# Optimization experiments

Hardware: AMD Instinct MI355X
Metric: run time of the kernel (lower is better)

Reference implementation:

```python
import jax, jax.numpy as jnp
import numpy as np

SEMA_DIM = 1024
L1, L2, B = 256, 320, 64


def setup_inputs() -> dict:
    key = jax.random.key(0)
    k1, k2, kw1, kb1, kw2, kb2 = jax.random.split(key, 6)
    D = SEMA_DIM
    s = 1.0 / np.sqrt(D)
    return {
        "r1": jax.random.normal(k1, (L1, B, D), dtype=jnp.float32),
        "r2": jax.random.normal(k2, (L2, B, D), dtype=jnp.float32),
        "W1": jax.random.uniform(kw1, (D, D), jnp.float32, -s, s),
        "b1": jax.random.uniform(kb1, (D,), jnp.float32, -s, s),
        "W2": jax.random.uniform(kw2, (D, D), jnp.float32, -s, s),
        "b2": jax.random.uniform(kb2, (D,), jnp.float32, -s, s),
    }


def _mlp(x, W1, b1, W2, b2):
    # torch Linear: x @ W.T + b
    h = jax.nn.relu(x @ W1.T + b1)
    return h @ W2.T + b2


def reference(r1, r2, W1, b1, W2, b2):
    # (L, B, D) -> mlp -> (B, L, D)
    r1 = jnp.transpose(_mlp(r1, W1, b1, W2, b2), (1, 0, 2))  # [B, L1, D]
    r2 = jnp.transpose(_mlp(r2, W1, b1, W2, b2), (1, 0, 2))  # [B, L2, D]

    o = jnp.einsum("bid,bjd->bij", r1, r2)  # [B, L1, L2]
    o1 = jax.nn.softmax(o, axis=2)           # attend r1 -> r2
    o2 = jax.nn.softmax(o, axis=1)           # attend r2 -> r1

    r1_c = jnp.einsum("bij,bjd->bid", o1, r2)  # [B, L1, D]
    r2_c = jnp.einsum("bij,bid->bjd", o2, r1)  # [B, L2, D]

    r1_pool = jnp.concatenate([r1, r1_c], axis=-1).sum(axis=1) / r1.shape[1]  # [B, 2D]
    r2_pool = jnp.concatenate([r2, r2_c], axis=-1).sum(axis=1) / r2.shape[1]  # [B, 2D]
    return (r1_pool, r2_pool)
```

## Files before the change

kernel.cpp:

```cpp
#include <hip/hip_runtime.h>
#include <stdint.h>

#define L1C 256
#define L2C 320
#define BC  64
#define DC  1024

typedef __bf16 bf16_t;
typedef __bf16 bf16x8 __attribute__((ext_vector_type(8)));
typedef __bf16 bf16x4 __attribute__((ext_vector_type(4)));
typedef float  f32x4  __attribute__((ext_vector_type(4)));

__device__ __forceinline__ void gload16(const void* g, void* l) {
  __builtin_amdgcn_global_load_lds(
      (__attribute__((address_space(1))) void*)g,
      (__attribute__((address_space(3))) void*)l, 16, 0, 0);
}

__global__ __launch_bounds__(256)
void conv_kernel(const float* __restrict__ src, bf16_t* __restrict__ dst, int n4) {
  int i = blockIdx.x * 256 + threadIdx.x;
  const int stride = gridDim.x * 256;
  for (; i < n4; i += stride) {
    float4 v = ((const float4*)src)[i];
    bf16x4 o = { (__bf16)v.x, (__bf16)v.y, (__bf16)v.z, (__bf16)v.w };
    ((bf16x4*)dst)[i] = o;
  }
}

__global__ __launch_bounds__(256)
void w2t_kernel(const float* __restrict__ W2, bf16_t* __restrict__ W2T) {
  __shared__ float tile[32][33];
  const int tx = threadIdx.x & 31, ty = threadIdx.x >> 5;
  const int x0 = blockIdx.x * 32, y0 = blockIdx.y * 32;
#pragma unroll
  for (int k = 0; k < 32; k += 8)
    tile[ty + k][tx] = W2[(size_t)(y0 + ty + k) * 1024 + x0 + tx];
  __syncthreads();
#pragma unroll
  for (int k = 0; k < 32; k += 8)
    W2T[(size_t)(x0 + ty + k) * 1024 + y0 + tx] = (bf16_t)tile[tx][ty + k];
}

__global__ __launch_bounds__(256)
void wb_kernel(const float* __restrict__ W2, const float* __restrict__ b2,
               float* __restrict__ w2b) {
  const int dt = threadIdx.x & 15, kg = threadIdx.x >> 4;
  const int d = blockIdx.x * 16 + dt;
  float s = 0.f;
  for (int k = kg * 64; k < kg * 64 + 64; ++k)
    s += W2[(size_t)k * 1024 + d] * b2[k];
  __shared__ float red[16][17];
  red[kg][dt] = s;
  __syncthreads();
  if (kg == 0) {
    float t = 0.f;
#pragma unroll
    for (int g = 0; g < 16; ++g) t += red[g][dt];
    w2b[d] = t;
  }
}

__global__ __launch_bounds__(512, 2)
void mlp_gemm8(const bf16_t* __restrict__ A, const bf16_t* __restrict__ W,
               const float* __restrict__ bias, bf16_t* __restrict__ C,
               int Mtiles, int relu) {
  const int nwg = Mtiles * 4;
  const int cpx = nwg >> 3;
  const int wg  = ((int)blockIdx.x & 7) * cpx + ((int)blockIdx.x >> 3);
  const int mt = wg >> 2, nt = wg & 3;

  __shared__ __align__(16) char lds[131072];

  const int t    = threadIdx.x;
  const int lane = t & 63, wid = t >> 6;
  const int wm = wid >> 2, wn = wid & 3;
  const int rsel = lane & 15, hi = lane >> 4;
  const int t16 = t * 16;

  const int P0 = t16, P1 = 8192 + t16;
  const int Lg0 = P0 ^ ((P0 >> 3) & 0x30);
  const int Lg1 = P1 ^ ((P1 >> 3) & 0x30);
  const int rS0 = Lg0 >> 6, cS0 = (Lg0 & 63) >> 1;
  const int rS1 = Lg1 >> 6, cS1 = (Lg1 & 63) >> 1;
  const bf16_t* pA0 = A + (size_t)(mt * 256 + rS0) * 1024 + cS0;
  const bf16_t* pA1 = A + (size_t)(mt * 256 + rS1) * 1024 + cS1;
  const bf16_t* pB0 = W + (size_t)(nt * 256 + rS0) * 1024 + cS0;
  const bf16_t* pB1 = W + (size_t)(nt * 256 + rS1) * 1024 + cS1;

  const int kchunk = (hi ^ ((rsel >> 1) & 3)) << 4;
  const int offA = ((wm * 128 + rsel) << 6) + kchunk;
  const int offB = 16384 + ((wn * 64 + rsel) << 6) + kchunk;

  f32x4 acc[8][4] = {};
  bf16x8 bfr[4];

#pragma unroll
  for (int p = 0; p < 3; ++p) {
    char* db = lds + p * 32768;
    gload16(pA0 + p * 32, db + t16);
    gload16(pA1 + p * 32, db + 8192 + t16);
    gload16(pB0 + p * 32, db + 16384 + t16);
    gload16(pB1 + p * 32, db + 24576 + t16);
  }
  asm volatile("s_waitcnt vmcnt(8)" ::: "memory");
  __builtin_amdgcn_s_barrier();
  __builtin_amdgcn_sched_barrier(0);

#pragma unroll 1
  for (int tt = 0; tt < 32; ++tt) {
    const char* rb = lds + (tt & 3) * 32768;
    char* sb = lds + ((tt + 3) & 3) * 32768;
    const int ks = (tt + 3) * 32;
    bf16x8 af[4];
#pragma unroll
    for (int m = 0; m < 4; ++m) af[m] = *(const bf16x8*)(rb + offA + m * 1024);
#pragma unroll
    for (int n = 0; n < 4; ++n) bfr[n] = *(const bf16x8*)(rb + offB + n * 1024);
    if (tt < 29) {
      gload16(pA0 + ks, sb + t16);
      gload16(pA1 + ks, sb + 8192 + t16);
    }
    __builtin_amdgcn_s_setprio(1);
#pragma unroll
    for (int m = 0; m < 4; ++m)
#pragma unroll
      for (int n = 0; n < 4; ++n)
        acc[m][n] = __builtin_amdgcn_mfma_f32_16x16x32_bf16(af[m], bfr[n], acc[m][n], 0, 0, 0);
    __builtin_amdgcn_s_setprio(0);
    __builtin_amdgcn_s_barrier();
    __builtin_amdgcn_sched_barrier(0);
#pragma unroll
    for (int m = 0; m < 4; ++m) af[m] = *(const bf16x8*)(rb + offA + (m + 4) * 1024);
    if (tt < 29) {
      gload16(pB0 + ks, sb + 16384 + t16);
      gload16(pB1 + ks, sb + 24576 + t16);
    }
    __builtin_amdgcn_s_setprio(1);
#pragma unroll
    for (int m = 0; m < 4; ++m)
#pragma unroll
      for (int n = 0; n < 4; ++n)
        acc[m + 4][n] = __builtin_amdgcn_mfma_f32_16x16x32_bf16(af[m], bfr[n], acc[m + 4][n], 0, 0, 0);
    __builtin_amdgcn_s_setprio(0);
    if (tt < 29)       asm volatile("s_waitcnt vmcnt(8)" ::: "memory");
    else if (tt == 29) asm volatile("s_waitcnt vmcnt(4)" ::: "memory");
    else if (tt == 30) asm volatile("s_waitcnt vmcnt(0)" ::: "memory");
    __builtin_amdgcn_s_barrier();
    __builtin_amdgcn_sched_barrier(0);
  }

  const int row0 = mt * 256 + wm * 128 + hi * 4;
  const int col0 = nt * 256 + wn * 64 + rsel;
  float bv[4];
#pragma unroll
  for (int n = 0; n < 4; ++n) bv[n] = bias[col0 + n * 16];
#pragma unroll
  for (int m = 0; m < 8; ++m) {
#pragma unroll
    for (int q = 0; q < 4; ++q) {
      const size_t rr = (size_t)(row0 + m * 16 + q) * 1024;
#pragma unroll
      for (int n = 0; n < 4; ++n) {
        float v = acc[m][n][q] + bv[n];
        if (relu) v = fmaxf(v, 0.f);
        C[rr + col0 + n * 16] = (bf16_t)v;
      }
    }
  }
}

__global__ __launch_bounds__(256)
void mlp_gemm(const bf16_t* __restrict__ A, const bf16_t* __restrict__ W,
              const float* __restrict__ bias, bf16_t* __restrict__ C,
              int Mtiles, int relu) {
  const int nwg = Mtiles * 8;
  const int wg  = ((int)blockIdx.x & 7) * (nwg >> 3) + ((int)blockIdx.x >> 3);
  const int mt = wg >> 3, nt = wg & 7;

  const int f = threadIdx.x;
  const int lane = f & 63, w = f >> 6;
  const int sRow = f >> 2, sCol8 = (f & 3) * 8;

  const bf16_t* Ab = A + (size_t)mt * 128 * 1024 + (size_t)sRow * 1024 + sCol8;
  const bf16_t* Bb = W + (size_t)nt * 128 * 1024 + (size_t)sRow * 1024 + sCol8;

  __shared__ __align__(16) bf16_t sA[128 * 32];
  __shared__ __align__(16) bf16_t sB[128 * 32];
  bf16_t* sAp = sA + sRow * 32 + sCol8;
  bf16_t* sBp = sB + sRow * 32 + sCol8;

  const int wr = (w >> 1) * 64, wc = (w & 1) * 64;
  const int rsel = lane & 15, koff = (lane >> 4) * 8;
  const bf16_t* rA = sA + (wr + rsel) * 32 + koff;
  const bf16_t* rB = sB + (wc + rsel) * 32 + koff;

  f32x4 acc[4][4] = {};
  for (int kt = 0; kt < 1024; kt += 32) {
    __syncthreads();
    gload16(Ab + kt,             sAp);
    gload16(Ab + kt + 64 * 1024, sAp + 64 * 32);
    gload16(Bb + kt,             sBp);
    gload16(Bb + kt + 64 * 1024, sBp + 64 * 32);
    asm volatile("s_waitcnt vmcnt(0)" ::: "memory");
    __syncthreads();
    bf16x8 af[4], bfv[4];
#pragma unroll
    for (int m = 0; m < 4; ++m) af[m] = *(const bf16x8*)(rA + m * 16 * 32);
#pragma unroll
    for (int n = 0; n < 4; ++n) bfv[n] = *(const bf16x8*)(rB + n * 16 * 32);
#pragma unroll
    for (int m = 0; m < 4; ++m)
#pragma unroll
      for (int n = 0; n < 4; ++n)
        acc[m][n] = __builtin_amdgcn_mfma_f32_16x16x32_bf16(af[m], bfv[n], acc[m][n], 0, 0, 0);
  }

  const int row0 = mt * 128 + wr + (lane >> 4) * 4;
  const int col0 = nt * 128 + wc + rsel;
#pragma unroll
  for (int n = 0; n < 4; ++n) {
    const int c = col0 + n * 16;
    const float bv = bias[c];
#pragma unroll
    for (int m = 0; m < 4; ++m) {
      const int r = row0 + m * 16;
#pragma unroll
      for (int q = 0; q < 4; ++q) {
        float v = acc[m][n][q] + bv;
        if (relu) v = fmaxf(v, 0.f);
        C[(size_t)(r + q) * 1024 + c] = (bf16_t)v;
      }
    }
  }
}

__global__ __launch_bounds__(256)
void pool_gemm(const bf16_t* __restrict__ A, const bf16_t* __restrict__ W,
               const float* __restrict__ bias, float* __restrict__ out) {
  const int nwg = 16;
  const int wg  = ((int)blockIdx.x & 7) * (nwg >> 3) + ((int)blockIdx.x >> 3);
  const int mt = wg >> 3, nt = wg & 7;

  const int f = threadIdx.x;
  const int lane = f & 63, w = f >> 6;
  const int sRow = f >> 2, sCol8 = (f & 3) * 8;

  const bf16_t* Ab = A + (size_t)mt * 128 * 1024 + (size_t)sRow * 1024 + sCol8;
  const bf16_t* Bb = W + (size_t)nt * 128 * 1024 + (size_t)sRow * 1024 + sCol8;

  __shared__ __align__(16) bf16_t sA[128 * 32];
  __shared__ __align__(16) bf16_t sB[128 * 32];
  bf16_t* sAp = sA + sRow * 32 + sCol8;
  bf16_t* sBp = sB + sRow * 32 + sCol8;

  const int wr = (w >> 1) * 64, wc = (w & 1) * 64;
  const int rsel = lane & 15, koff = (lane >> 4) * 8;
  const bf16_t* rA = sA + (wr + rsel) * 32 + koff;
  const bf16_t* rB = sB + (wc + rsel) * 32 + koff;

  f32x4 acc[4][4] = {};
  for (int kt = 0; kt < 1024; kt += 32) {
    __syncthreads();
    gload16(Ab + kt,             sAp);
    gload16(Ab + kt + 64 * 1024, sAp + 64 * 32);
    gload16(Bb + kt,             sBp);
    gload16(Bb + kt + 64 * 1024, sBp + 64 * 32);
    asm volatile("s_waitcnt vmcnt(0)" ::: "memory");
    __syncthreads();
    bf16x8 af[4], bfv[4];
#pragma unroll
    for (int m = 0; m < 4; ++m) af[m] = *(const bf16x8*)(rA + m * 16 * 32);
#pragma unroll
    for (int n = 0; n < 4; ++n) bfv[n] = *(const bf16x8*)(rB + n * 16 * 32);
#pragma unroll
    for (int m = 0; m < 4; ++m)
#pragma unroll
      for (int n = 0; n < 4; ++n)
        acc[m][n] = __builtin_amdgcn_mfma_f32_16x16x32_bf16(af[m], bfv[n], acc[m][n], 0, 0, 0);
  }

  const int row0 = mt * 128 + wr + (lane >> 4) * 4;
  const int col0 = nt * 128 + wc + rsel;
#pragma unroll
  for (int n = 0; n < 4; ++n) {
    const int c = col0 + n * 16;
    const float bv = bias[c];
#pragma unroll
    for (int m = 0; m < 4; ++m) {
      const int r = row0 + m * 16;
#pragma unroll
      for (int q = 0; q < 4; ++q) {
        const int rg = r + q;
        const size_t oo = (size_t)(rg >> 7) * 131072 + (size_t)(rg & 63) * 2048 +
                          ((rg >> 6) & 1) * 1024 + c;
        out[oo] = acc[m][n][q] + bv;
      }
    }
  }
}

__global__ __launch_bounds__(256)
void t_kernel(const bf16_t* __restrict__ H, const float* __restrict__ w2b,
              float* __restrict__ tT1, float* __restrict__ tT2) {
  const int wv = threadIdx.x >> 6, lane = threadIdx.x & 63;
  const int r = blockIdx.x * 4 + wv;
  const bf16_t* hrow = H + (size_t)r * 1024;
  float s = 0.f;
#pragma unroll
  for (int h = 0; h < 2; ++h) {
    bf16x8 v = *(const bf16x8*)(hrow + h * 512 + lane * 8);
#pragma unroll
    for (int e = 0; e < 8; ++e) s += (float)v[e] * w2b[h * 512 + lane * 8 + e];
  }
#pragma unroll
  for (int off = 32; off; off >>= 1) s += __shfl_xor(s, off);
  if (lane == 0) {
    const int b = r & 63;
    if (r < 16384) tT1[b * L1C + (r >> 6)] = s;
    else           tT2[b * L2C + ((r - 16384) >> 6)] = s;
  }
}

__global__ __launch_bounds__(256)
void logits_gemm(const bf16_t* __restrict__ Y1, const bf16_t* __restrict__ Y2,
                 float* __restrict__ O) {
  const int wg = ((int)blockIdx.x & 7) * 48 + ((int)blockIdx.x >> 3);
  const int b = wg / 6, t = wg % 6;
  const int mt = t / 3, nt = t % 3;

  const int f = threadIdx.x;
  const int lane = f & 63, w = f >> 6;
  const int sRow = f >> 2, sCol8 = (f & 3) * 8;

  const int i0 = mt * 128 + sRow;
  const int i1 = i0 + 64;
  int j0 = nt * 128 + sRow;      if (j0 > L2C - 1) j0 = L2C - 1;
  int j1 = nt * 128 + sRow + 64; if (j1 > L2C - 1) j1 = L2C - 1;
  const bf16_t* A0 = Y1 + ((size_t)i0 * BC + b) * DC + sCol8;
  const bf16_t* A1 = Y1 + ((size_t)i1 * BC + b) * DC + sCol8;
  const bf16_t* B0 = Y2 + ((size_t)j0 * BC + b) * DC + sCol8;
  const bf16_t* B1 = Y2 + ((size_t)j1 * BC + b) * DC + sCol8;

  __shared__ __align__(16) bf16_t sA[128 * 32];
  __shared__ __align__(16) bf16_t sB[128 * 32];
  bf16_t* sAp = sA + sRow * 32 + sCol8;
  bf16_t* sBp = sB + sRow * 32 + sCol8;

  const int wr = (w >> 1) * 64, wc = (w & 1) * 64;
  const int rsel = lane & 15, koff = (lane >> 4) * 8;
  const bf16_t* rA = sA + (wr + rsel) * 32 + koff;
  const bf16_t* rB = sB + (wc + rsel) * 32 + koff;

  f32x4 acc[4][4] = {};
  for (int kt = 0; kt < 1024; kt += 32) {
    __syncthreads();
    gload16(A0 + kt, sAp);
    gload16(A1 + kt, sAp + 64 * 32);
    gload16(B0 + kt, sBp);
    gload16(B1 + kt, sBp + 64 * 32);
    asm volatile("s_waitcnt vmcnt(0)" ::: "memory");
    __syncthreads();
    bf16x8 af[4], bfv[4];
#pragma unroll
    for (int m = 0; m < 4; ++m) af[m] = *(const bf16x8*)(rA + m * 16 * 32);
#pragma unroll
    for (int n = 0; n < 4; ++n) bfv[n] = *(const bf16x8*)(rB + n * 16 * 32);
#pragma unroll
    for (int m = 0; m < 4; ++m)
#pragma unroll
      for (int n = 0; n < 4; ++n)
        acc[m][n] = __builtin_amdgcn_mfma_f32_16x16x32_bf16(af[m], bfv[n], acc[m][n], 0, 0, 0);
  }

  float* Ob = O + (size_t)b * L1C * L2C;
  const int row0 = mt * 128 + wr + (lane >> 4) * 4;
  const int col0 = nt * 128 + wc + rsel;
#pragma unroll
  for (int n = 0; n < 4; ++n) {
    const int c = col0 + n * 16;
    if (c < L2C) {
#pragma unroll
      for (int m = 0; m < 4; ++m) {
        const int r = row0 + m * 16;
#pragma unroll
        for (int q = 0; q < 4; ++q)
          Ob[(size_t)(r + q) * L2C + c] = acc[m][n][q];
      }
    }
  }
}

__global__ __launch_bounds__(256)
void row_stats(const float* __restrict__ O, const float* __restrict__ tT2,
               float* __restrict__ rowM, float* __restrict__ rowInv) {
  const int gw = blockIdx.x * 4 + (threadIdx.x >> 6);
  const int lane = threadIdx.x & 63;
  const int b = gw >> 8;
  const float* row = O + (size_t)gw * L2C;
  const float* t2 = tT2 + b * L2C;
  float v[5];
  float m = -1e30f;
#pragma unroll
  for (int t = 0; t < 5; ++t) { v[t] = row[t * 64 + lane] + t2[t * 64 + lane]; m = fmaxf(m, v[t]); }
#pragma unroll
  for (int off = 32; off; off >>= 1) m = fmaxf(m, __shfl_xor(m, off));
  float s = 0.f;
#pragma unroll
  for (int t = 0; t < 5; ++t) s += __expf(v[t] - m);
#pragma unroll
  for (int off = 32; off; off >>= 1) s += __shfl_xor(s, off);
  if (lane == 0) { rowM[gw] = m; rowInv[gw] = 1.f / s; }
}

__global__ __launch_bounds__(256)
void col_stats_c1(const float* __restrict__ O, const float* __restrict__ tT1,
                  const float* __restrict__ tT2,
                  const float* __restrict__ rowM, const float* __restrict__ rowInv,
                  float* __restrict__ colM, float* __restrict__ colInv,
                  float* __restrict__ c1) {
  const int b = blockIdx.x / 5, jb = blockIdx.x % 5;
  const int jl = threadIdx.x & 63, ig = threadIdx.x >> 6;
  const int j = jb * 64 + jl;
  const float* Ob = O + (size_t)b * L1C * L2C + j;
  const float* rM = rowM + b * L1C;
  const float* rI = rowInv + b * L1C;
  const float* t1 = tT1 + b * L1C;
  const float t2j = tT2[b * L2C + j];
  float m = -1e30f, s = 0.f, cp = 0.f;
  for (int i = ig; i < L1C; i += 4) {
    float ov = Ob[(size_t)i * L2C];
    float v = ov + t1[i];
    float mn = fmaxf(m, v);
    s = s * __expf(m - mn) + __expf(v - mn);
    m = mn;
    cp += __expf(ov + t2j - rM[i]) * rI[i];
  }
  __shared__ float sm[4][64], ss[4][64], sc[4][64];
  sm[ig][jl] = m; ss[ig][jl] = s; sc[ig][jl] = cp;
  __syncthreads();
  if (ig == 0) {
    for (int g = 1; g < 4; ++g) {
      float mg = sm[g][jl], sg = ss[g][jl];
      float mn = fmaxf(m, mg);
      s = s * __expf(m - mn) + sg * __expf(mg - mn);
      m = mn;
      cp += sc[g][jl];
    }
    colM[b * L2C + j] = m;
    colInv[b * L2C + j] = 1.f / s;
    c1[b * L2C + j] = cp;
  }
}

__global__ __launch_bounds__(256)
void c2_kernel(const float* __restrict__ O, const float* __restrict__ tT1,
               const float* __restrict__ colM, const float* __restrict__ colInv,
               float* __restrict__ c2) {
  const int gw = blockIdx.x * 4 + (threadIdx.x >> 6);
  const int lane = threadIdx.x & 63;
  const int b = gw >> 8;
  const float* row = O + (size_t)gw * L2C;
  const float* cM = colM + b * L2C;
  const float* cI = colInv + b * L2C;
  const float t1i = tT1[b * L1C + (gw & 255)];
  float s = 0.f;
#pragma unroll
  for (int t = 0; t < 5; ++t) {
    const int j = t * 64 + lane;
    s += __expf(row[j] + t1i - cM[j]) * cI[j];
  }
#pragma unroll
  for (int off = 32; off; off >>= 1) s += __shfl_xor(s, off);
  if (lane == 0) c2[gw] = s;
}

__global__ __launch_bounds__(256)
void u_kernel(const bf16_t* __restrict__ H, const float* __restrict__ c1,
              const float* __restrict__ c2, bf16_t* __restrict__ Ub) {
  const int b = blockIdx.x >> 2;
  const int d = (blockIdx.x & 3) * 256 + threadIdx.x;
  const bf16_t* H2 = H + (size_t)L1C * BC * DC;
  float s1 = 0.f, s1c = 0.f, s2 = 0.f, s2c = 0.f;
  const float* c2b = c2 + b * L1C;
  for (int i = 0; i < L1C; ++i) {
    float v = (float)H[((size_t)i * BC + b) * DC + d];
    s1 += v; s1c += c2b[i] * v;
  }
  const float* c1b = c1 + b * L2C;
  for (int j = 0; j < L2C; ++j) {
    float v = (float)H2[((size_t)j * BC + b) * DC + d];
    s2 += v; s2c += c1b[j] * v;
  }
  Ub[(size_t)(0 * 64 + b) * 1024 + d] = (bf16_t)(s1  * (1.f / L1C));
  Ub[(size_t)(1 * 64 + b) * 1024 + d] = (bf16_t)(s2c * (1.f / L1C));
  Ub[(size_t)(2 * 64 + b) * 1024 + d] = (bf16_t)(s2  * (1.f / L2C));
  Ub[(size_t)(3 * 64 + b) * 1024 + d] = (bf16_t)(s1c * (1.f / L2C));
}

extern "C" void kernel_launch(void* const* d_in, const int* in_sizes, int n_in,
                              void* d_out, int out_size, void* d_ws, size_t ws_size,
                              hipStream_t stream) {
  const float* r1 = (const float*)d_in[0];
  const float* r2 = (const float*)d_in[1];
  const float* W1 = (const float*)d_in[2];
  const float* b1 = (const float*)d_in[3];
  const float* W2 = (const float*)d_in[4];
  const float* b2 = (const float*)d_in[5];
  float* out = (float*)d_out;
  char* ws = (char*)d_ws;

  const size_t M1 = (size_t)L1C * BC;
  const size_t M2 = (size_t)L2C * BC;
  const size_t Mt = M1 + M2;

  size_t off = 0;
  bf16_t* XB  = (bf16_t*)(ws + off); off += Mt * DC * 2;
  bf16_t* HB  = (bf16_t*)(ws + off); off += Mt * DC * 2;
  bf16_t* WB1 = (bf16_t*)(ws + off); off += (size_t)DC * DC * 2;
  bf16_t* WB2 = (bf16_t*)(ws + off); off += (size_t)DC * DC * 2;
  bf16_t* W2T = (bf16_t*)(ws + off); off += (size_t)DC * DC * 2;
  bf16_t* GB  = (bf16_t*)(ws + off); off += (size_t)DC * DC * 2;
  float* w2b   = (float*)(ws + off); off += 4096;
  float* zb    = (float*)(ws + off); off += 4096;
  float* tT1   = (float*)(ws + off); off += BC * L1C * 4;
  float* tT2   = (float*)(ws + off); off += BC * L2C * 4;
  float* rowM  = (float*)(ws + off); off += BC * L1C * 4;
  float* rowIv = (float*)(ws + off); off += BC * L1C * 4;
  float* colM  = (float*)(ws + off); off += BC * L2C * 4;
  float* colIv = (float*)(ws + off); off += BC * L2C * 4;
  float* c1v   = (float*)(ws + off); off += BC * L2C * 4;
  float* c2v   = (float*)(ws + off); off += BC * L1C * 4;
  bf16_t* Ub   = (bf16_t*)(ws + off); off += 256 * DC * 2;

  bf16_t* Z = XB;
  float*  O = (float*)((char*)XB + 35651584);
  bf16_t* H2 = HB + M1 * DC;

  conv_kernel<<<2048, 256, 0, stream>>>(r1, XB,           (int)(M1 * DC / 4));
  conv_kernel<<<2048, 256, 0, stream>>>(r2, XB + M1 * DC, (int)(M2 * DC / 4));
  conv_kernel<<<512,  256, 0, stream>>>(W1, WB1, (int)((size_t)DC * DC / 4));
  conv_kernel<<<512,  256, 0, stream>>>(W2, WB2, (int)((size_t)DC * DC / 4));
  w2t_kernel<<<dim3(32, 32), 256, 0, stream>>>(W2, W2T);
  wb_kernel<<<64, 256, 0, stream>>>(W2, b2, w2b);
  hipMemsetAsync(zb, 0, 4096, stream);

  mlp_gemm8<<<576, 512, 0, stream>>>(XB, WB1, b1, HB, 144, 1);

  mlp_gemm<<<64, 256, 0, stream>>>(W2T, W2T, zb, GB, 8, 0);
  t_kernel<<<9216, 256, 0, stream>>>(HB, w2b, tT1, tT2);

  mlp_gemm8<<<256, 512, 0, stream>>>(HB, GB, zb, Z, 64, 0);

  logits_gemm<<<384, 256, 0, stream>>>(Z, H2, O);

  row_stats<<<4096, 256, 0, stream>>>(O, tT2, rowM, rowIv);
  col_stats_c1<<<320, 256, 0, stream>>>(O, tT1, tT2, rowM, rowIv, colM, colIv, c1v);
  c2_kernel<<<4096, 256, 0, stream>>>(O, tT1, colM, colIv, c2v);

  u_kernel<<<256, 256, 0, stream>>>(HB, c1v, c2v, Ub);
  pool_gemm<<<16, 256, 0, stream>>>(Ub, WB2, b2, out);
}
```

Baseline: 330.7 us.

## Split-K small GEMMs and fuse row-dot t computation into first MLP GEMM epilogue

The W2ᵀW2 Gram GEMM (64 workgroups) and the pooling GEMM (16 workgroups) both badly under-fill the GPU, so each is split along K into slices that write fp32 partials, followed by a small reduce kernel that sums the slices and applies bias and layout. The separate t_kernel, which reread H to dot each row with w2b, is removed. That dot product is now computed in the first MLP GEMM epilogue with shuffles and atomicAdd into zeroed tT buffers. The trade-offs are extra partial-buffer traffic, additional launches and memsets, atomic contention, and non-deterministic summation order.

```diff
diff --git a/kernel.cpp b/kernel.cpp
--- a/kernel.cpp
+++ b/kernel.cpp
@@ -64,7 +64,8 @@
 __global__ __launch_bounds__(512, 2)
 void mlp_gemm8(const bf16_t* __restrict__ A, const bf16_t* __restrict__ W,
                const float* __restrict__ bias, bf16_t* __restrict__ C,
-               int Mtiles, int relu) {
+               int Mtiles, int relu, const float* __restrict__ w2b,
+               float* __restrict__ tT1, float* __restrict__ tT2) {
   const int nwg = Mtiles * 4;
   const int cpx = nwg >> 3;
   const int wg  = ((int)blockIdx.x & 7) * cpx + ((int)blockIdx.x >> 3);
@@ -168,15 +169,47 @@
       }
     }
   }
-}
-
-__global__ __launch_bounds__(256)
-void mlp_gemm(const bf16_t* __restrict__ A, const bf16_t* __restrict__ W,
-              const float* __restrict__ bias, bf16_t* __restrict__ C,
-              int Mtiles, int relu) {
-  const int nwg = Mtiles * 8;
-  const int wg  = ((int)blockIdx.x & 7) * (nwg >> 3) + ((int)blockIdx.x >> 3);
-  const int mt = wg >> 3, nt = wg & 7;
+
+  if (w2b) {
+    float wv[4];
+#pragma unroll
+    for (int n = 0; n < 4; ++n) wv[n] = w2b[col0 + n * 16];
+#pragma unroll
+    for (int m = 0; m < 8; ++m) {
+#pragma unroll
+      for (int q = 0; q < 4; ++q) {
+        float s = 0.f;
+#pragma unroll
+        for (int n = 0; n < 4; ++n) {
+          float v = acc[m][n][q] + bv[n];
+          if (relu) v = fmaxf(v, 0.f);
+          v = (float)(bf16_t)v;
+          s += v * wv[n];
+        }
+        s += __shfl_xor(s, 1);
+        s += __shfl_xor(s, 2);
+        s += __shfl_xor(s, 4);
+        s += __shfl_xor(s, 8);
+        if (rsel == 0) {
+          const int r = row0 + m * 16 + q;
+          if (r < 16384) atomicAdd(&tT1[(r & 63) * L1C + (r >> 6)], s);
+          else {
+            const int r2 = r - 16384;
+            atomicAdd(&tT2[(r2 & 63) * L2C + (r2 >> 6)], s);
+          }
+        }
+      }
+    }
+  }
+}
+
+__global__ __launch_bounds__(256)
+void gemmK(const bf16_t* __restrict__ A, const bf16_t* __restrict__ W,
+           float* __restrict__ P, int KS) {
+  const int slice = (int)blockIdx.x >> 6;
+  const int tl = (int)blockIdx.x & 63;
+  const int mt = tl >> 3, nt = tl & 7;
+  const int koff = slice * KS;
 
   const int f = threadIdx.x;
   const int lane = f & 63, w = f >> 6;
@@ -191,12 +224,12 @@
   bf16_t* sBp = sB + sRow * 32 + sCol8;
 
   const int wr = (w >> 1) * 64, wc = (w & 1) * 64;
-  const int rsel = lane & 15, koff = (lane >> 4) * 8;
-  const bf16_t* rA = sA + (wr + rsel) * 32 + koff;
-  const bf16_t* rB = sB + (wc + rsel) * 32 + koff;
+  const int rsel = lane & 15, koff2 = (lane >> 4) * 8;
+  const bf16_t* rA = sA + (wr + rsel) * 32 + koff2;
+  const bf16_t* rB = sB + (wc + rsel) * 32 + koff2;
 
   f32x4 acc[4][4] = {};
-  for (int kt = 0; kt < 1024; kt += 32) {
+  for (int kt = koff; kt < koff + KS; kt += 32) {
     __syncthreads();
     gload16(Ab + kt,             sAp);
     gload16(Ab + kt + 64 * 1024, sAp + 64 * 32);
@@ -216,31 +249,41 @@
         acc[m][n] = __builtin_amdgcn_mfma_f32_16x16x32_bf16(af[m], bfv[n], acc[m][n], 0, 0, 0);
   }
 
+  float* Pb = P + (size_t)slice * 1048576;
   const int row0 = mt * 128 + wr + (lane >> 4) * 4;
   const int col0 = nt * 128 + wc + rsel;
 #pragma unroll
   for (int n = 0; n < 4; ++n) {
     const int c = col0 + n * 16;
-    const float bv = bias[c];
 #pragma unroll
     for (int m = 0; m < 4; ++m) {
       const int r = row0 + m * 16;
 #pragma unroll
-      for (int q = 0; q < 4; ++q) {
-        float v = acc[m][n][q] + bv;
-        if (relu) v = fmaxf(v, 0.f);
-        C[(size_t)(r + q) * 1024 + c] = (bf16_t)v;
-      }
-    }
-  }
-}
-
-__global__ __launch_bounds__(256)
-void pool_gemm(const bf16_t* __restrict__ A, const bf16_t* __restrict__ W,
-               const float* __restrict__ bias, float* __restrict__ out) {
-  const int nwg = 16;
-  const int wg  = ((int)blockIdx.x & 7) * (nwg >> 3) + ((int)blockIdx.x >> 3);
-  const int mt = wg >> 3, nt = wg & 7;
+      for (int q = 0; q < 4; ++q)
+        Pb[(size_t)(r + q) * 1024 + c] = acc[m][n][q];
+    }
+  }
+}
+
+__global__ __launch_bounds__(256)
+void g_reduce(const float* __restrict__ Gp, bf16_t* __restrict__ GB) {
+  const int i4 = blockIdx.x * 256 + threadIdx.x;
+  float4 a = ((const float4*)Gp)[i4];
+  float4 b = ((const float4*)(Gp + 1048576))[i4];
+  float4 c = ((const float4*)(Gp + 2097152))[i4];
+  float4 d = ((const float4*)(Gp + 3145728))[i4];
+  bf16x4 o = { (bf16_t)(a.x + b.x + c.x + d.x), (bf16_t)(a.y + b.y + c.y + d.y),
+               (bf16_t)(a.z + b.z + c.z + d.z), (bf16_t)(a.w + b.w + c.w + d.w) };
+  ((bf16x4*)GB)[i4] = o;
+}
+
+__global__ __launch_bounds__(256)
+void pool_gemmK(const bf16_t* __restrict__ A, const bf16_t* __restrict__ W,
+                float* __restrict__ P) {
+  const int slice = (int)blockIdx.x >> 4;
+  const int tl = (int)blockIdx.x & 15;
+  const int mt = tl >> 3, nt = tl & 7;
+  const int koff = slice * 128;
 
   const int f = threadIdx.x;
   const int lane = f & 63, w = f >> 6;
@@ -255,12 +298,12 @@
   bf16_t* sBp = sB + sRow * 32 + sCol8;
 
   const int wr = (w >> 1) * 64, wc = (w & 1) * 64;
-  const int rsel = lane & 15, koff = (lane >> 4) * 8;
-  const bf16_t* rA = sA + (wr + rsel) * 32 + koff;
-  const bf16_t* rB = sB + (wc + rsel) * 32 + koff;
+  const int rsel = lane & 15, koff2 = (lane >> 4) * 8;
+  const bf16_t* rA = sA + (wr + rsel) * 32 + koff2;
+  const bf16_t* rB = sB + (wc + rsel) * 32 + koff2;
 
   f32x4 acc[4][4] = {};
-  for (int kt = 0; kt < 1024; kt += 32) {
+  for (int kt = koff; kt < koff + 128; kt += 32) {
     __syncthreads();
     gload16(Ab + kt,             sAp);
     gload16(Ab + kt + 64 * 1024, sAp + 64 * 32);
@@ -280,46 +323,32 @@
         acc[m][n] = __builtin_amdgcn_mfma_f32_16x16x32_bf16(af[m], bfv[n], acc[m][n], 0, 0, 0);
   }
 
+  float* Pb = P + (size_t)slice * 262144;
   const int row0 = mt * 128 + wr + (lane >> 4) * 4;
   const int col0 = nt * 128 + wc + rsel;
 #pragma unroll
   for (int n = 0; n < 4; ++n) {
     const int c = col0 + n * 16;
-    const float bv = bias[c];
 #pragma unroll
     for (int m = 0; m < 4; ++m) {
       const int r = row0 + m * 16;
 #pragma unroll
-      for (int q = 0; q < 4; ++q) {
-        const int rg = r + q;
-        const size_t oo = (size_t)(rg >> 7) * 131072 + (size_t)(rg & 63) * 2048 +
-                          ((rg >> 6) & 1) * 1024 + c;
-        out[oo] = acc[m][n][q] + bv;
-      }
-    }
-  }
-}
-
-__global__ __launch_bounds__(256)
-void t_kernel(const bf16_t* __restrict__ H, const float* __restrict__ w2b,
-              float* __restrict__ tT1, float* __restrict__ tT2) {
-  const int wv = threadIdx.x >> 6, lane = threadIdx.x & 63;
-  const int r = blockIdx.x * 4 + wv;
-  const bf16_t* hrow = H + (size_t)r * 1024;
-  float s = 0.f;
-#pragma unroll
-  for (int h = 0; h < 2; ++h) {
-    bf16x8 v = *(const bf16x8*)(hrow + h * 512 + lane * 8);
-#pragma unroll
-    for (int e = 0; e < 8; ++e) s += (float)v[e] * w2b[h * 512 + lane * 8 + e];
-  }
-#pragma unroll
-  for (int off = 32; off; off >>= 1) s += __shfl_xor(s, off);
-  if (lane == 0) {
-    const int b = r & 63;
-    if (r < 16384) tT1[b * L1C + (r >> 6)] = s;
-    else           tT2[b * L2C + ((r - 16384) >> 6)] = s;
-  }
+      for (int q = 0; q < 4; ++q)
+        Pb[(size_t)(r + q) * 1024 + c] = acc[m][n][q];
+    }
+  }
+}
+
+__global__ __launch_bounds__(256)
+void pool_reduce(const float* __restrict__ Pp, const float* __restrict__ b2,
+                 float* __restrict__ out) {
+  const int idx = blockIdx.x * 256 + threadIdx.x;
+  const int r = idx >> 10, c = idx & 1023;
+  float s = b2[c];
+#pragma unroll
+  for (int sl = 0; sl < 8; ++sl) s += Pp[(size_t)sl * 262144 + idx];
+  const int g = r >> 6, b = r & 63;
+  out[(size_t)(g >> 1) * 131072 + (size_t)b * 2048 + (g & 1) * 1024 + c] = s;
 }
 
 __global__ __launch_bounds__(256)
@@ -535,6 +564,8 @@
 
   bf16_t* Z = XB;
   float*  O = (float*)((char*)XB + 35651584);
+  float*  Gpart = (float*)((char*)XB + 58720256);
+  float*  Ppart = (float*)HB;
   bf16_t* H2 = HB + M1 * DC;
 
   conv_kernel<<<2048, 256, 0, stream>>>(r1, XB,           (int)(M1 * DC / 4));
@@ -544,13 +575,15 @@
   w2t_kernel<<<dim3(32, 32), 256, 0, stream>>>(W2, W2T);
   wb_kernel<<<64, 256, 0, stream>>>(W2, b2, w2b);
   hipMemsetAsync(zb, 0, 4096, stream);
-
-  mlp_gemm8<<<576, 512, 0, stream>>>(XB, WB1, b1, HB, 144, 1);
-
-  mlp_gemm<<<64, 256, 0, stream>>>(W2T, W2T, zb, GB, 8, 0);
-  t_kernel<<<9216, 256, 0, stream>>>(HB, w2b, tT1, tT2);
-
-  mlp_gemm8<<<256, 512, 0, stream>>>(HB, GB, zb, Z, 64, 0);
+  hipMemsetAsync(tT1, 0, BC * L1C * 4, stream);
+  hipMemsetAsync(tT2, 0, BC * L2C * 4, stream);
+
+  mlp_gemm8<<<576, 512, 0, stream>>>(XB, WB1, b1, HB, 144, 1, w2b, tT1, tT2);
+
+  gemmK<<<256, 256, 0, stream>>>(W2T, W2T, Gpart, 256);
+  g_reduce<<<1024, 256, 0, stream>>>(Gpart, GB);
+
+  mlp_gemm8<<<256, 512, 0, stream>>>(HB, GB, zb, Z, 64, 0, nullptr, nullptr, nullptr);
 
   logits_gemm<<<384, 256, 0, stream>>>(Z, H2, O);
 
@@ -559,5 +592,6 @@
   c2_kernel<<<4096, 256, 0, stream>>>(O, tT1, colM, colIv, c2v);
 
   u_kernel<<<256, 256, 0, stream>>>(HB, c1v, c2v, Ub);
-  pool_gemm<<<16, 256, 0, stream>>>(Ub, WB2, b2, out);
-}
+  pool_gemmK<<<128, 256, 0, stream>>>(Ub, WB2, Ppart);
+  pool_reduce<<<1024, 256, 0, stream>>>(Ppart, b2, out);
+}
```

After: 336.4 us. No clear change (+1.7%).
